# Performance work log

Hardware: AMD Instinct MI355X
Metric: run time of the kernel (lower is better)

## Reference

```python
import jax, jax.numpy as jnp
import numpy as np

VOCAB, D, A = 50000, 200, 32
R, L, B, NNZ = 30000, 40, 10000, 300000


def setup_inputs() -> dict:
    key = jax.random.key(0)
    ks = jax.random.split(key, 12)
    historical_review = jax.random.randint(ks[0], (R, L), 0, VOCAB)
    review_positive = jax.random.normal(ks[1], (R, D), jnp.float32)
    review_negative = jax.random.normal(ks[2], (R, D), jnp.float32)
    u_rows = jax.random.randint(ks[3], (1, NNZ), 0, B)
    u_cols = jax.random.randint(ks[4], (1, NNZ), 0, R)
    user_histor_index = jnp.concatenate([u_rows, u_cols], axis=0)
    user_histor_value = jax.random.uniform(ks[5], (NNZ,), jnp.float32)
    i_rows = jax.random.randint(ks[6], (1, NNZ), 0, B)
    i_cols = jax.random.randint(ks[7], (1, NNZ), 0, R)
    item_histor_index = jnp.concatenate([i_rows, i_cols], axis=0)
    item_histor_value = jax.random.uniform(ks[8], (NNZ,), jnp.float32)
    # parameters (torch nn.Linear convention: y = x @ W.T + b)
    emb_table = jax.random.normal(ks[9], (VOCAB, D), jnp.float32) * 0.1  # frozen
    W_M = jax.random.normal(ks[10], (D, D), jnp.float32) / np.sqrt(D)
    W_W = jax.random.normal(ks[11], (A, D), jnp.float32) / np.sqrt(D)
    b_W = jnp.zeros((A,), jnp.float32)
    return {
        "historical_review": historical_review,
        "review_positive": review_positive,
        "review_negative": review_negative,
        "user_histor_index": user_histor_index,
        "user_histor_value": user_histor_value,
        "item_histor_index": item_histor_index,
        "item_histor_value": item_histor_value,
        "batch_size": B,
        "emb_table": emb_table,
        "W_M": W_M,
        "W_W": W_W,
        "b_W": b_W,
    }


def _spmm(index, value, p_t, n_rows):
    # sparse [n_rows, R] @ p_t [R, A] via gather + segment-sum
    rows, cols = index[0], index[1]
    contrib = value[:, None] * p_t[cols]  # [nnz, A]
    return jax.ops.segment_sum(contrib, rows, num_segments=n_rows)


def reference(historical_review, review_positive, review_negative,
              user_histor_index, user_histor_value,
              item_histor_index, item_histor_value,
              batch_size, emb_table, W_M, W_W, b_W):
    e_w = emb_table[historical_review]                    # [R, L, D] gather
    # dx = matmul(transform_M(e_w), y_s[...,None]) -> [R, L]
    mew = jnp.einsum('rld,ed->rle', e_w, W_M)             # transform_M
    dx = jnp.einsum('rld,rd->rl', mew, review_positive)
    ax = jax.nn.softmax(dx, axis=1)                       # softmax over words
    z_s = jnp.einsum('rld,rl->rd', e_w, ax)               # attention pooling
    p_t = z_s @ W_W.T + b_W                               # [R, A]
    user_aspect = _spmm(user_histor_index, user_histor_value, p_t, batch_size)
    item_aspect = _spmm(item_histor_index, item_histor_value, p_t, batch_size)
    return (user_aspect, item_aspect)
```

## Files before the change

kernel.cpp:

```cpp
#include <hip/hip_runtime.h>
#include <math.h>

#define VOCAB 50000
#define DD 200
#define AA 32
#define RR 30000
#define LL 40
#define BB 10000

typedef _Float16 half2_t __attribute__((ext_vector_type(2)));

static __device__ __forceinline__ unsigned short f2h(float f) {
    return __builtin_bit_cast(unsigned short, (_Float16)f);
}
static __device__ __forceinline__ float hlo(unsigned int u) {
    return (float)__builtin_bit_cast(_Float16, (unsigned short)(u & 0xFFFFu));
}
static __device__ __forceinline__ float hhi(unsigned int u) {
    return (float)__builtin_bit_cast(_Float16, (unsigned short)(u >> 16));
}
static __device__ __forceinline__ unsigned int pkh(float lo, float hi) {
    return (unsigned int)f2h(lo) | ((unsigned int)f2h(hi) << 16);
}
static __device__ __forceinline__ float dot2(unsigned int a, unsigned int b, float acc) {
#if __has_builtin(__builtin_amdgcn_fdot2)
    return __builtin_amdgcn_fdot2(__builtin_bit_cast(half2_t, a),
                                  __builtin_bit_cast(half2_t, b), acc, false);
#else
    return acc + hlo(a) * hlo(b) + hhi(a) * hhi(b);
#endif
}

#define NC4 (VOCAB * DD / 4)
#define NWM ((DD / 2) * DD)
#define NWW (AA * (DD / 2))
__global__ __launch_bounds__(256) void prep_kernel(
    const float* __restrict__ emb, const float* __restrict__ WM,
    const float* __restrict__ WW, unsigned short* __restrict__ emb16,
    unsigned int* __restrict__ WMP, unsigned int* __restrict__ WWP)
{
    int i = blockIdx.x * 256 + threadIdx.x;
    if (i < NC4) {
        float4 f = ((const float4*)emb)[i];
        ushort4 u;
        u.x = f2h(f.x); u.y = f2h(f.y); u.z = f2h(f.z); u.w = f2h(f.w);
        ((ushort4*)emb16)[i] = u;
    } else if (i < NC4 + NWM) {
        int k = i - NC4;
        int e2 = k / DD, d = k - e2 * DD;
        WMP[k] = pkh(WM[(2 * e2) * DD + d], WM[(2 * e2 + 1) * DD + d]);
    } else if (i < NC4 + NWM + NWW) {
        int k = i - NC4 - NWM;
        int a = k / (DD / 2), c = k - a * (DD / 2);
        WWP[k] = pkh(WW[a * DD + 2 * c], WW[a * DD + 2 * c + 1]);
    }
}

__global__ __launch_bounds__(256) void v_gemm_kernel(
    const float* __restrict__ Y, const unsigned int* __restrict__ WMP,
    unsigned int* __restrict__ V16)
{
    __shared__ unsigned int yt[32 * (DD / 2)];
    const int r0 = blockIdx.x * 32;
    const int tid = threadIdx.x;

    for (int i = tid; i < 32 * 50; i += 256) {
        int j = i / 50, c = i - 50 * j;
        int r = r0 + j;
        float4 f = (r < RR) ? ((const float4*)(Y + (size_t)r * DD))[c]
                            : make_float4(0.f, 0.f, 0.f, 0.f);
        uint2 u = make_uint2(pkh(f.x, f.y), pkh(f.z, f.w));
        ((uint2*)yt)[i] = u;
    }
    __syncthreads();

    if (tid < DD) {
        float acc[32];
        #pragma unroll
        for (int j = 0; j < 32; ++j) acc[j] = 0.f;
        for (int e2 = 0; e2 < DD / 2; e2 += 2) {
            unsigned int w0 = WMP[e2 * DD + tid];
            unsigned int w1 = WMP[(e2 + 1) * DD + tid];
            #pragma unroll
            for (int j = 0; j < 32; ++j) {
                uint2 y2 = *(const uint2*)(yt + j * (DD / 2) + e2);
                acc[j] = dot2(y2.x, w0, acc[j]);
                acc[j] = dot2(y2.y, w1, acc[j]);
            }
        }
        #pragma unroll
        for (int j = 0; j < 32; ++j) {
            float partner = __shfl_xor(acc[j], 1);
            int r = r0 + j;
            if (r < RR && (tid & 1) == 0)
                V16[(size_t)r * (DD / 2) + (tid >> 1)] =
                    pkh(acc[j], partner);
        }
    }
}

__global__ __launch_bounds__(256, 8) void attn_kernel(
    const int* __restrict__ hist, const unsigned short* __restrict__ emb16,
    const unsigned int* __restrict__ V16, const unsigned int* __restrict__ WWP,
    const float* __restrict__ bW, float* __restrict__ PT)
{
    __shared__ __align__(16) unsigned short ew[LL * DD];
    __shared__ __align__(16) unsigned int vp[DD / 2];
    __shared__ float zss[4][DD];
    __shared__ float sws[4];
    __shared__ __align__(16) unsigned int zsp[DD / 2];

    const int r = blockIdx.x;
    const int tid = threadIdx.x;
    const int* hrow = hist + r * LL;

    const int i0 = tid, i1 = tid + 256, i2 = tid + 512, i3 = tid + 768;
    const int l0 = i0 / 25, c0 = i0 - 25 * l0;
    const int l1 = i1 / 25, c1 = i1 - 25 * l1;
    const int l2 = i2 / 25, c2 = i2 - 25 * l2;
    const int l3 = i3 / 25, c3 = i3 - 25 * l3;
    const bool has3 = (i3 < LL * 25);

    int w0 = hrow[l0];
    int w1 = hrow[l1];
    int w2 = hrow[l2];
    int w3 = has3 ? hrow[l3] : 0;

    uint4 q0 = ((const uint4*)(emb16 + (size_t)w0 * DD))[c0];
    uint4 q1 = ((const uint4*)(emb16 + (size_t)w1 * DD))[c1];
    uint4 q2 = ((const uint4*)(emb16 + (size_t)w2 * DD))[c2];
    uint4 q3 = has3 ? ((const uint4*)(emb16 + (size_t)w3 * DD))[c3]
                    : make_uint4(0u, 0u, 0u, 0u);
    uint4 vv = make_uint4(0u, 0u, 0u, 0u);
    if (tid < 25) vv = ((const uint4*)(V16 + (size_t)r * (DD / 2)))[tid];

    ((uint4*)ew)[i0] = q0;
    ((uint4*)ew)[i1] = q1;
    ((uint4*)ew)[i2] = q2;
    if (has3) ((uint4*)ew)[i3] = q3;
    if (tid < 25) ((uint4*)vp)[tid] = vv;
    __syncthreads();

    const int wave = tid >> 6, lane = tid & 63;
    const int half = lane >> 5, s = lane & 31;
    const bool act = (s < 25);

    uint4 vq = act ? ((const uint4*)vp)[s] : make_uint4(0u, 0u, 0u, 0u);

    half2_t zp0 = (half2_t)0, zp1 = (half2_t)0, zp2 = (half2_t)0, zp3 = (half2_t)0;
    float sw = 0.f;
    #pragma unroll 1
    for (int j = 0; j < 5; ++j) {
        const int l = wave * 10 + 2 * j + half;
        float p = 0.f;
        uint4 eq = make_uint4(0u, 0u, 0u, 0u);
        if (act) {
            eq = *(const uint4*)(ew + l * DD + s * 8);
            p = dot2(eq.x, vq.x, p);
            p = dot2(eq.y, vq.y, p);
            p = dot2(eq.z, vq.z, p);
            p = dot2(eq.w, vq.w, p);
        }
        #pragma unroll
        for (int off = 16; off; off >>= 1) p += __shfl_xor(p, off);
        float wgt = __expf(p - 4.0f);
        _Float16 wh = (_Float16)wgt;
        half2_t w2v; w2v[0] = wh; w2v[1] = wh;
        sw += (float)wh;
        zp0 = __builtin_bit_cast(half2_t, eq.x) * w2v + zp0;
        zp1 = __builtin_bit_cast(half2_t, eq.y) * w2v + zp1;
        zp2 = __builtin_bit_cast(half2_t, eq.z) * w2v + zp2;
        zp3 = __builtin_bit_cast(half2_t, eq.w) * w2v + zp3;
    }

    float z0 = (float)zp0[0], z1 = (float)zp0[1];
    float z2 = (float)zp1[0], z3 = (float)zp1[1];
    float z4 = (float)zp2[0], z5 = (float)zp2[1];
    float z6 = (float)zp3[0], z7 = (float)zp3[1];
    z0 += __shfl_xor(z0, 32); z1 += __shfl_xor(z1, 32);
    z2 += __shfl_xor(z2, 32); z3 += __shfl_xor(z3, 32);
    z4 += __shfl_xor(z4, 32); z5 += __shfl_xor(z5, 32);
    z6 += __shfl_xor(z6, 32); z7 += __shfl_xor(z7, 32);
    float swt = sw + __shfl_xor(sw, 32);
    if (half == 0 && act) {
        ((float4*)zss[wave])[2 * s]     = make_float4(z0, z1, z2, z3);
        ((float4*)zss[wave])[2 * s + 1] = make_float4(z4, z5, z6, z7);
    }
    if (lane == 0) sws[wave] = swt;
    __syncthreads();

    if (tid < DD / 2) {
        float tot = sws[0] + sws[1] + sws[2] + sws[3];
        int d = 2 * tid;
        float za = (zss[0][d]     + zss[1][d]     + zss[2][d]     + zss[3][d])     / tot;
        float zb = (zss[0][d + 1] + zss[1][d + 1] + zss[2][d + 1] + zss[3][d + 1]) / tot;
        zsp[tid] = pkh(za, zb);
    }
    __syncthreads();

    {
        int a = tid >> 3, j = tid & 7;
        float acc = 0.f;
        #pragma unroll
        for (int k = 0; k < 13; ++k) {
            int c = j + 8 * k;
            if (c < DD / 2) acc = dot2(zsp[c], WWP[a * (DD / 2) + c], acc);
        }
        #pragma unroll
        for (int off = 4; off; off >>= 1) acc += __shfl_xor(acc, off);
        if (j == 0) PT[r * AA + a] = acc + bW[a];
    }
}

__global__ __launch_bounds__(256) void spmm_kernel(
    const int* __restrict__ uidx, const float* __restrict__ uval,
    const int* __restrict__ iidx, const float* __restrict__ ival,
    const float* __restrict__ PT, float* __restrict__ out, int nnz)
{
    int g = blockIdx.x * 256 + threadIdx.x;
    int grp = g >> 5;
    int a = g & 31;
    const int gpm = (nnz + 3) >> 2;
    const int* idx = uidx;
    const float* val = uval;
    float* o = out;
    if (grp >= gpm) {
        grp -= gpm;
        if (grp >= gpm) return;
        idx = iidx; val = ival; o += BB * AA;
    }
    const int n0 = grp * 4;

    if (((nnz & 3) == 0) && (n0 + 4 <= nnz)) {
        int4   rows = *(const int4*)(idx + n0);
        int4   cols = *(const int4*)(idx + nnz + n0);
        float4 ws   = *(const float4*)(val + n0);
        atomicAdd(&o[rows.x * AA + a], ws.x * PT[cols.x * AA + a]);
        atomicAdd(&o[rows.y * AA + a], ws.y * PT[cols.y * AA + a]);
        atomicAdd(&o[rows.z * AA + a], ws.z * PT[cols.z * AA + a]);
        atomicAdd(&o[rows.w * AA + a], ws.w * PT[cols.w * AA + a]);
    } else {
        for (int k = 0; k < 4; ++k) {
            int n = n0 + k;
            if (n >= nnz) break;
            int row = idx[n];
            int col = idx[nnz + n];
            float w = val[n];
            atomicAdd(&o[row * AA + a], w * PT[col * AA + a]);
        }
    }
}

extern "C" void kernel_launch(void* const* d_in, const int* in_sizes, int n_in,
                              void* d_out, int out_size, void* d_ws, size_t ws_size,
                              hipStream_t stream) {
    const int*   hist = (const int*)d_in[0];
    const float* ypos = (const float*)d_in[1];
    const int*   uidx = (const int*)d_in[3];
    const float* uval = (const float*)d_in[4];
    const int*   iidx = (const int*)d_in[5];
    const float* ival = (const float*)d_in[6];
    const float* emb  = (const float*)d_in[8];
    const float* WM   = (const float*)d_in[9];
    const float* WW   = (const float*)d_in[10];
    const float* bW   = (const float*)d_in[11];

    unsigned short* emb16 = (unsigned short*)d_ws;
    unsigned int* WMP = (unsigned int*)(emb16 + (size_t)VOCAB * DD);
    unsigned int* WWP = WMP + NWM;
    unsigned int* V16 = WWP + NWW;
    float* PT = (float*)(V16 + (size_t)RR * (DD / 2));
    float* out = (float*)d_out;

    const int nnz = in_sizes[4];

    hipMemsetAsync(d_out, 0, (size_t)out_size * sizeof(float), stream);

    prep_kernel<<<(NC4 + NWM + NWW + 255) / 256, 256, 0, stream>>>(
        emb, WM, WW, emb16, WMP, WWP);
    v_gemm_kernel<<<(RR + 31) / 32, 256, 0, stream>>>(ypos, WMP, V16);
    attn_kernel<<<RR, 256, 0, stream>>>(hist, emb16, V16, WWP, bW, PT);

    const int gpm = (nnz + 3) >> 2;
    const int spmm_blocks = (2 * gpm * 32 + 255) / 256;
    spmm_kernel<<<spmm_blocks, 256, 0, stream>>>(uidx, uval, iidx, ival, PT, out, nnz);
}
```

Before: 227.5 us.

## Precompute vocab-level aspect projection and pool projected embeddings in attention

```diff
diff --git a/kernel.cpp b/kernel.cpp
--- a/kernel.cpp
+++ b/kernel.cpp
@@ -56,6 +56,41 @@
     }
 }
 
+__global__ __launch_bounds__(256) void ew_gemm_kernel(
+    const unsigned short* __restrict__ emb16, const unsigned int* __restrict__ WWP,
+    float* __restrict__ EW)
+{
+    __shared__ unsigned int et[32][DD / 2];
+    __shared__ unsigned int wwT[DD / 2][AA];
+    const int r0 = blockIdx.x * 32;
+    const int tid = threadIdx.x;
+
+    for (int i = tid; i < AA * (DD / 2); i += 256) {
+        int a = i / (DD / 2), c = i - a * (DD / 2);
+        wwT[c][a] = WWP[i];
+    }
+    for (int i = tid; i < 32 * 25; i += 256) {
+        int rl = i / 25, c4 = i - rl * 25;
+        int r = r0 + rl;
+        ((uint4*)et[rl])[c4] = (r < VOCAB)
+            ? ((const uint4*)(emb16 + (size_t)r * DD))[c4]
+            : make_uint4(0u, 0u, 0u, 0u);
+    }
+    __syncthreads();
+
+    const int a = tid & 31, rg = tid >> 5;
+    #pragma unroll
+    for (int k = 0; k < 4; ++k) {
+        int rl = rg + 8 * k;
+        float acc = 0.f;
+        #pragma unroll 4
+        for (int c = 0; c < DD / 2; ++c)
+            acc = dot2(et[rl][c], wwT[c][a], acc);
+        int r = r0 + rl;
+        if (r < VOCAB) EW[(size_t)r * AA + a] = acc;
+    }
+}
+
 __global__ __launch_bounds__(256) void v_gemm_kernel(
     const float* __restrict__ Y, const unsigned int* __restrict__ WMP,
     unsigned int* __restrict__ V16)
@@ -101,14 +136,13 @@
 
 __global__ __launch_bounds__(256, 8) void attn_kernel(
     const int* __restrict__ hist, const unsigned short* __restrict__ emb16,
-    const unsigned int* __restrict__ V16, const unsigned int* __restrict__ WWP,
+    const unsigned int* __restrict__ V16, const float* __restrict__ EW,
     const float* __restrict__ bW, float* __restrict__ PT)
 {
     __shared__ __align__(16) unsigned short ew[LL * DD];
     __shared__ __align__(16) unsigned int vp[DD / 2];
-    __shared__ float zss[4][DD];
+    __shared__ float accs[4][AA];
     __shared__ float sws[4];
-    __shared__ __align__(16) unsigned int zsp[DD / 2];
 
     const int r = blockIdx.x;
     const int tid = threadIdx.x;
@@ -146,16 +180,16 @@
     const bool act = (s < 25);
 
     uint4 vq = act ? ((const uint4*)vp)[s] : make_uint4(0u, 0u, 0u, 0u);
-
-    half2_t zp0 = (half2_t)0, zp1 = (half2_t)0, zp2 = (half2_t)0, zp3 = (half2_t)0;
+    int h = (lane < LL) ? hrow[lane] : 0;
+
+    float pa = 0.f;
     float sw = 0.f;
     #pragma unroll 1
     for (int j = 0; j < 5; ++j) {
         const int l = wave * 10 + 2 * j + half;
         float p = 0.f;
-        uint4 eq = make_uint4(0u, 0u, 0u, 0u);
         if (act) {
-            eq = *(const uint4*)(ew + l * DD + s * 8);
+            uint4 eq = *(const uint4*)(ew + l * DD + s * 8);
             p = dot2(eq.x, vq.x, p);
             p = dot2(eq.y, vq.y, p);
             p = dot2(eq.z, vq.z, p);
@@ -163,52 +197,22 @@
         }
         #pragma unroll
         for (int off = 16; off; off >>= 1) p += __shfl_xor(p, off);
-        float wgt = __expf(p - 4.0f);
-        _Float16 wh = (_Float16)wgt;
-        half2_t w2v; w2v[0] = wh; w2v[1] = wh;
-        sw += (float)wh;
-        zp0 = __builtin_bit_cast(half2_t, eq.x) * w2v + zp0;
-        zp1 = __builtin_bit_cast(half2_t, eq.y) * w2v + zp1;
-        zp2 = __builtin_bit_cast(half2_t, eq.z) * w2v + zp2;
-        zp3 = __builtin_bit_cast(half2_t, eq.w) * w2v + zp3;
-    }
-
-    float z0 = (float)zp0[0], z1 = (float)zp0[1];
-    float z2 = (float)zp1[0], z3 = (float)zp1[1];
-    float z4 = (float)zp2[0], z5 = (float)zp2[1];
-    float z6 = (float)zp3[0], z7 = (float)zp3[1];
-    z0 += __shfl_xor(z0, 32); z1 += __shfl_xor(z1, 32);
-    z2 += __shfl_xor(z2, 32); z3 += __shfl_xor(z3, 32);
-    z4 += __shfl_xor(z4, 32); z5 += __shfl_xor(z5, 32);
-    z6 += __shfl_xor(z6, 32); z7 += __shfl_xor(z7, 32);
+        float wgt = __expf(p - 8.0f);
+        sw += wgt;
+        int wi = __shfl(h, l);
+        pa += wgt * EW[(size_t)wi * AA + s];
+    }
+
+    pa += __shfl_xor(pa, 32);
     float swt = sw + __shfl_xor(sw, 32);
-    if (half == 0 && act) {
-        ((float4*)zss[wave])[2 * s]     = make_float4(z0, z1, z2, z3);
-        ((float4*)zss[wave])[2 * s + 1] = make_float4(z4, z5, z6, z7);
-    }
+    if (half == 0) accs[wave][s] = pa;
     if (lane == 0) sws[wave] = swt;
     __syncthreads();
 
-    if (tid < DD / 2) {
+    if (tid < AA) {
         float tot = sws[0] + sws[1] + sws[2] + sws[3];
-        int d = 2 * tid;
-        float za = (zss[0][d]     + zss[1][d]     + zss[2][d]     + zss[3][d])     / tot;
-        float zb = (zss[0][d + 1] + zss[1][d + 1] + zss[2][d + 1] + zss[3][d + 1]) / tot;
-        zsp[tid] = pkh(za, zb);
-    }
-    __syncthreads();
-
-    {
-        int a = tid >> 3, j = tid & 7;
-        float acc = 0.f;
-        #pragma unroll
-        for (int k = 0; k < 13; ++k) {
-            int c = j + 8 * k;
-            if (c < DD / 2) acc = dot2(zsp[c], WWP[a * (DD / 2) + c], acc);
-        }
-        #pragma unroll
-        for (int off = 4; off; off >>= 1) acc += __shfl_xor(acc, off);
-        if (j == 0) PT[r * AA + a] = acc + bW[a];
+        float t = accs[0][tid] + accs[1][tid] + accs[2][tid] + accs[3][tid];
+        PT[r * AA + tid] = t / tot + bW[tid];
     }
 }
 
@@ -270,6 +274,7 @@
     unsigned int* WWP = WMP + NWM;
     unsigned int* V16 = WWP + NWW;
     float* PT = (float*)(V16 + (size_t)RR * (DD / 2));
+    float* EW = PT + (size_t)RR * AA;
     float* out = (float*)d_out;
 
     const int nnz = in_sizes[4];
@@ -278,8 +283,9 @@
 
     prep_kernel<<<(NC4 + NWM + NWW + 255) / 256, 256, 0, stream>>>(
         emb, WM, WW, emb16, WMP, WWP);
+    ew_gemm_kernel<<<(VOCAB + 31) / 32, 256, 0, stream>>>(emb16, WWP, EW);
     v_gemm_kernel<<<(RR + 31) / 32, 256, 0, stream>>>(ypos, WMP, V16);
-    attn_kernel<<<RR, 256, 0, stream>>>(hist, emb16, V16, WWP, bW, PT);
+    attn_kernel<<<RR, 256, 0, stream>>>(hist, emb16, V16, EW, bW, PT);
 
     const int gpm = (nnz + 3) >> 2;
     const int spmm_blocks = (2 * gpm * 32 + 255) / 256;
```

Measured after the change: 257.5 us. +13.2%, slower.

## Privatize SpMM atomic outputs into copies and switch attention pooling to fp32

Applied to the files above, without the earlier changes.

```diff
diff --git a/kernel.cpp b/kernel.cpp
--- a/kernel.cpp
+++ b/kernel.cpp
@@ -7,6 +7,7 @@
 #define RR 30000
 #define LL 40
 #define BB 10000
+#define NPRIV 4
 
 typedef _Float16 half2_t __attribute__((ext_vector_type(2)));
 
@@ -147,7 +148,8 @@
 
     uint4 vq = act ? ((const uint4*)vp)[s] : make_uint4(0u, 0u, 0u, 0u);
 
-    half2_t zp0 = (half2_t)0, zp1 = (half2_t)0, zp2 = (half2_t)0, zp3 = (half2_t)0;
+    float z0 = 0.f, z1 = 0.f, z2 = 0.f, z3 = 0.f,
+          z4 = 0.f, z5 = 0.f, z6 = 0.f, z7 = 0.f;
     float sw = 0.f;
     #pragma unroll 1
     for (int j = 0; j < 5; ++j) {
@@ -163,20 +165,14 @@
         }
         #pragma unroll
         for (int off = 16; off; off >>= 1) p += __shfl_xor(p, off);
-        float wgt = __expf(p - 4.0f);
-        _Float16 wh = (_Float16)wgt;
-        half2_t w2v; w2v[0] = wh; w2v[1] = wh;
-        sw += (float)wh;
-        zp0 = __builtin_bit_cast(half2_t, eq.x) * w2v + zp0;
-        zp1 = __builtin_bit_cast(half2_t, eq.y) * w2v + zp1;
-        zp2 = __builtin_bit_cast(half2_t, eq.z) * w2v + zp2;
-        zp3 = __builtin_bit_cast(half2_t, eq.w) * w2v + zp3;
-    }
-
-    float z0 = (float)zp0[0], z1 = (float)zp0[1];
-    float z2 = (float)zp1[0], z3 = (float)zp1[1];
-    float z4 = (float)zp2[0], z5 = (float)zp2[1];
-    float z6 = (float)zp3[0], z7 = (float)zp3[1];
+        float wgt = __expf(p - 8.0f);
+        sw += wgt;
+        z0 += wgt * hlo(eq.x); z1 += wgt * hhi(eq.x);
+        z2 += wgt * hlo(eq.y); z3 += wgt * hhi(eq.y);
+        z4 += wgt * hlo(eq.z); z5 += wgt * hhi(eq.z);
+        z6 += wgt * hlo(eq.w); z7 += wgt * hhi(eq.w);
+    }
+
     z0 += __shfl_xor(z0, 32); z1 += __shfl_xor(z1, 32);
     z2 += __shfl_xor(z2, 32); z3 += __shfl_xor(z3, 32);
     z4 += __shfl_xor(z4, 32); z5 += __shfl_xor(z5, 32);
@@ -215,7 +211,7 @@
 __global__ __launch_bounds__(256) void spmm_kernel(
     const int* __restrict__ uidx, const float* __restrict__ uval,
     const int* __restrict__ iidx, const float* __restrict__ ival,
-    const float* __restrict__ PT, float* __restrict__ out, int nnz)
+    const float* __restrict__ PT, float* __restrict__ outP, int nnz)
 {
     int g = blockIdx.x * 256 + threadIdx.x;
     int grp = g >> 5;
@@ -223,15 +219,16 @@
     const int gpm = (nnz + 3) >> 2;
     const int* idx = uidx;
     const float* val = uval;
-    float* o = out;
+    size_t obase = 0;
     if (grp >= gpm) {
         grp -= gpm;
         if (grp >= gpm) return;
-        idx = iidx; val = ival; o += BB * AA;
-    }
+        idx = iidx; val = ival; obase = (size_t)BB * AA;
+    }
+    float* o = outP + (size_t)(grp & (NPRIV - 1)) * (2 * BB * AA) + obase;
     const int n0 = grp * 4;
 
-    if (((nnz & 3) == 0) && (n0 + 4 <= nnz)) {
+    if (n0 + 4 <= nnz) {
         int4   rows = *(const int4*)(idx + n0);
         int4   cols = *(const int4*)(idx + nnz + n0);
         float4 ws   = *(const float4*)(val + n0);
@@ -251,6 +248,21 @@
     }
 }
 
+__global__ __launch_bounds__(256) void reduce_kernel(
+    const float* __restrict__ outP, float* __restrict__ out)
+{
+    const int N4 = 2 * BB * AA / 4;
+    int i = blockIdx.x * 256 + threadIdx.x;
+    if (i >= N4) return;
+    float4 s = ((const float4*)outP)[i];
+    #pragma unroll
+    for (int k = 1; k < NPRIV; ++k) {
+        float4 t = ((const float4*)(outP + (size_t)k * 2 * BB * AA))[i];
+        s.x += t.x; s.y += t.y; s.z += t.z; s.w += t.w;
+    }
+    ((float4*)out)[i] = s;
+}
+
 extern "C" void kernel_launch(void* const* d_in, const int* in_sizes, int n_in,
                               void* d_out, int out_size, void* d_ws, size_t ws_size,
                               hipStream_t stream) {
@@ -270,11 +282,12 @@
     unsigned int* WWP = WMP + NWM;
     unsigned int* V16 = WWP + NWW;
     float* PT = (float*)(V16 + (size_t)RR * (DD / 2));
+    float* outP = PT + (size_t)RR * AA;
     float* out = (float*)d_out;
 
     const int nnz = in_sizes[4];
 
-    hipMemsetAsync(d_out, 0, (size_t)out_size * sizeof(float), stream);
+    hipMemsetAsync(outP, 0, (size_t)NPRIV * 2 * BB * AA * sizeof(float), stream);
 
     prep_kernel<<<(NC4 + NWM + NWW + 255) / 256, 256, 0, stream>>>(
         emb, WM, WW, emb16, WMP, WWP);
@@ -283,5 +296,6 @@
 
     const int gpm = (nnz + 3) >> 2;
     const int spmm_blocks = (2 * gpm * 32 + 255) / 256;
-    spmm_kernel<<<spmm_blocks, 256, 0, stream>>>(uidx, uval, iidx, ival, PT, out, nnz);
-}
+    spmm_kernel<<<spmm_blocks, 256, 0, stream>>>(uidx, uval, iidx, ival, PT, outP, nnz);
+    reduce_kernel<<<(2 * BB * AA / 4 + 255) / 256, 256, 0, stream>>>(outP, out);
+}
```

Result: no change. 225.9 us (-0.7%).
